# Performance work log

Measured on AMD Instinct MI355X. Metric: run time of the kernel, lower is better.

Reference implementation:

```python
import jax, jax.numpy as jnp
import numpy as np

W_EDGE, W_LAP, W_NORMAL, W_VEL = 0.5, 0.05, 0.01, 10.0


def _grid_mesh(g):
    ids = np.arange(g * g).reshape(g, g)
    tl, tr = ids[:-1, :-1].ravel(), ids[:-1, 1:].ravel()
    bl, br = ids[1:, :-1].ravel(), ids[1:, 1:].ravel()
    f1 = np.stack([tl, bl, br], 1)
    f2 = np.stack([tl, br, tr], 1)
    return np.concatenate([f1, f2], 0).astype(np.int64)  # [F,3]


def _topology(faces):
    # all directed edges with the opposite vertex of their face
    e = np.concatenate([faces[:, [0, 1]], faces[:, [1, 2]], faces[:, [2, 0]]], 0)
    opp = np.concatenate([faces[:, 2], faces[:, 0], faces[:, 1]], 0)
    key = np.sort(e, axis=1)
    uniq, inv = np.unique(key, axis=0, return_inverse=True)  # unique undirected edges
    counts = np.bincount(inv)
    order = np.argsort(inv, kind='stable')
    sel = counts[inv[order]] == 2
    idx2 = order[sel].reshape(-1, 2)  # the two face-slots of each interior edge
    ekey = key[idx2[:, 0]]
    pairs = np.stack([ekey[:, 0], ekey[:, 1], opp[idx2[:, 0]], opp[idx2[:, 1]]], 1)
    return uniq.astype(np.int64), pairs.astype(np.int64)


def setup_inputs() -> dict:
    key = jax.random.key(0)
    k1, k2 = jax.random.split(key)
    B, g = 2, 91
    N = g * g  # 8281
    faces = _grid_mesh(g)                 # [16200,3]
    edges, nc_pairs = _topology(faces)    # [24480,2], [24120,4]
    predictions = jax.random.normal(k1, (B, N, 3), dtype=jnp.float32)
    targets = jax.random.normal(k2, (B, N, 3), dtype=jnp.float32)
    return {
        'predictions': predictions,
        'targets': targets,
        'pred_faces': jnp.asarray(faces),
        'edges': jnp.asarray(edges),
        'nc_pairs': jnp.asarray(nc_pairs),
    }


def _chamfer(x, y):
    # pytorch3d chamfer_distance: squared dists, point mean both ways, batch mean
    xx = jnp.sum(x * x, -1)
    yy = jnp.sum(y * y, -1)
    d = xx[:, :, None] + yy[:, None, :] - 2.0 * jnp.einsum('bnd,bmd->bnm', x, y)
    d = jnp.maximum(d, 0.0)
    return jnp.mean(jnp.min(d, axis=2).mean(axis=1) + jnp.min(d, axis=1).mean(axis=1))


def _edge_loss(verts, edges):
    # mean over meshes of mean over edges of squared edge length (target len 0)
    ve = verts[:, edges]  # [B,E,2,3]
    l2 = jnp.sum((ve[:, :, 0] - ve[:, :, 1]) ** 2, -1)
    return l2.mean()


def _cot_laplacian_loss_one(verts, faces):
    # verts [N,3]; pytorch3d cot_laplacian + method='cot' smoothing
    fv = verts[faces]  # [F,3,3]
    v0, v1, v2 = fv[:, 0], fv[:, 1], fv[:, 2]
    A = jnp.linalg.norm(v1 - v2, axis=1)
    Bl = jnp.linalg.norm(v0 - v2, axis=1)
    C = jnp.linalg.norm(v0 - v1, axis=1)
    s = 0.5 * (A + Bl + C)
    area = jnp.sqrt(jnp.maximum(s * (s - A) * (s - Bl) * (s - C), 1e-12))
    A2, B2, C2 = A * A, Bl * Bl, C * C
    cota = (B2 + C2 - A2) / area
    cotb = (A2 + C2 - B2) / area
    cotc = (A2 + B2 - C2) / area
    cot = jnp.stack([cota, cotb, cotc], 1) / 4.0  # [F,3]
    ii = faces[:, jnp.array([1, 2, 0])]
    jj = faces[:, jnp.array([2, 0, 1])]
    i = jnp.concatenate([ii, jj], 0).ravel()
    j = jnp.concatenate([jj, ii], 0).ravel()
    w = jnp.concatenate([cot, cot], 0).ravel()
    N = verts.shape[0]
    Lx = jnp.zeros_like(verts).at[i].add(w[:, None] * verts[j])
    rowsum = jnp.zeros((N,), dtype=verts.dtype).at[i].add(w)
    norm_w = jnp.where(rowsum > 0, 1.0 / rowsum, 0.0)
    res = Lx * norm_w[:, None] - verts
    return jnp.linalg.norm(res, axis=1).mean()


def _normal_consistency_one(verts, pairs):
    # pairs [P,4] = (v0, v1, opp_a, opp_b) per interior edge
    p = verts[pairs]  # [P,4,3]
    e = p[:, 1] - p[:, 0]
    n0 = jnp.cross(e, p[:, 2] - p[:, 0])
    n1 = -jnp.cross(e, p[:, 3] - p[:, 0])
    eps = 1e-8
    cos = jnp.sum(n0 * n1, -1) / (
        jnp.maximum(jnp.linalg.norm(n0, axis=1), eps)
        * jnp.maximum(jnp.linalg.norm(n1, axis=1), eps)
    )
    return (1.0 - cos).mean()


def _forward(predictions, targets, pred_faces, edges, nc_pairs):
    loss_cham = _chamfer(predictions, targets)
    edge_l = _edge_loss(predictions, edges)
    lap_l = jax.vmap(lambda v: _cot_laplacian_loss_one(v, pred_faces))(predictions).mean()
    nc_l = jax.vmap(lambda v: _normal_consistency_one(v, nc_pairs))(predictions).mean()
    pred_shift = predictions[:, 1:, :] - predictions[:, :-1, :]
    tgt_shift = targets[:, 1:, :] - targets[:, :-1, :]
    vel_l = _chamfer(pred_shift, tgt_shift)
    return loss_cham + W_LAP * lap_l + W_NORMAL * nc_l + W_EDGE * edge_l + W_VEL * vel_l


def reference(predictions, targets, pred_faces, edges, nc_pairs):
    return _forward(predictions, targets, pred_faces, edges, nc_pairs)
```

## Files before the change

### kernel.cpp

```cpp
#include <hip/hip_runtime.h>


typedef unsigned int uint32;
typedef __attribute__((ext_vector_type(8)))  short bf16x8;
typedef __attribute__((ext_vector_type(16))) float f32x16;

#define W_EDGE   0.5f
#define W_LAP    0.05f
#define W_NORMAL 0.01f
#define W_VEL    10.0f
#define BIGF     3.0e38f
#define RSTRIDE  8320

__device__ __forceinline__ unsigned short f2bf(float f){
    uint32 b = __float_as_uint(f);
    b += 0x7FFFu + ((b >> 16) & 1u);
    return (unsigned short)(b >> 16);
}
__device__ __forceinline__ float bf2f(unsigned short h){
    return __uint_as_float(((uint32)h) << 16);
}

__device__ __forceinline__ float wave_sum(float v) {
#pragma unroll
    for (int o = 32; o > 0; o >>= 1) v += __shfl_down(v, o, 64);
    return v;
}

__global__ void bprep_k(const float* __restrict__ pred, const float* __restrict__ tgt,
                        int N, uint4* __restrict__ bfrag,
                        float* __restrict__ ws, int nzero)
{
    {
        uint32* w = (uint32*)ws;
        for (int i = blockIdx.x * blockDim.x + threadIdx.x; i < nzero;
             i += gridDim.x * blockDim.x)
            w[i] = 0u;
    }

    const int NT = (N + 31) >> 5;
    const int gt = blockIdx.x * 4 + (threadIdx.x >> 6);
    if (gt >= 8 * NT) return;
    const int c = gt / NT, t = gt - c * NT;
    const int dir = c >> 2, ds = (c >> 1) & 1, b = c & 1;
    const int Np = N - ds;
    const int l = threadIdx.x & 63;
    const int col = t * 32 + (l & 31);
    const float* __restrict__ yb = (dir ? pred : tgt) + (size_t)b * N * 3;
    float y0 = 0.f, y1 = 0.f, y2 = 0.f;
    const bool valid = col < Np;
    if (valid){
        if (ds){
            y0 = yb[(col+1)*3+0] - yb[col*3+0];
            y1 = yb[(col+1)*3+1] - yb[col*3+1];
            y2 = yb[(col+1)*3+2] - yb[col*3+2];
        } else {
            y0 = yb[col*3+0]; y1 = yb[col*3+1]; y2 = yb[col*3+2];
        }
    }
    const float yy = fmaf(y0,y0, fmaf(y1,y1, y2*y2));
    unsigned short yh0=f2bf(y0), yh1=f2bf(y1), yh2=f2bf(y2);
    unsigned short yl0=f2bf(y0-bf2f(yh0)), yl1=f2bf(y1-bf2f(yh1)), yl2=f2bf(y2-bf2f(yh2));
    unsigned short yyh, yyl;
    if (valid){ yyh = f2bf(yy); yyl = f2bf(yy - bf2f(yyh)); }
    else      { yyh = f2bf(BIGF); yyl = 0; }
    const short ONE = (short)0x3F80;
    bf16x8 Bu;
    if (l < 32){
        Bu[0]=(short)yh0; Bu[1]=(short)yh1; Bu[2]=(short)yh2;
        Bu[3]=(short)yh0; Bu[4]=(short)yh1; Bu[5]=(short)yh2;
        Bu[6]=(short)yl0; Bu[7]=(short)yl1;
    } else {
        Bu[0]=(short)yl2; Bu[1]=ONE; Bu[2]=ONE; Bu[3]=(short)yyh; Bu[4]=(short)yyl;
        Bu[5]=0; Bu[6]=0; Bu[7]=0;
    }
    bfrag[(size_t)(c * NT + t) * 64 + l] = __builtin_bit_cast(uint4, Bu);
}

__global__ __launch_bounds__(256)
void mega_k(const float* __restrict__ pred, const float* __restrict__ tgt,
            int N, const uint4* __restrict__ bfrag, float* __restrict__ rowpart,
            const int* __restrict__ edges, int E,
            const int* __restrict__ pairs, int P,
            const int* __restrict__ faces, int F,
            int B, float scaleE, float scaleP,
            float* __restrict__ Lx, float* __restrict__ rowsum,
            float* __restrict__ accum)
{
    if (blockIdx.z == 8){
        const int tE = B * E, tP = B * P, tF = B * F;
        const int total = tE + tP + tF;
        const int bid = blockIdx.x * 4 + blockIdx.y;
        const int nthr = 260 * 256;
        float se = 0.f, sp = 0.f;
        for (int idx = bid * 256 + threadIdx.x; idx < total; idx += nthr) {
            if (idx < tE) {
                const int b = idx / E;
                const int e = idx - b * E;
                const float* __restrict__ vb = pred + (size_t)b * N * 3;
                const int i0 = edges[e * 2 + 0], i1 = edges[e * 2 + 1];
                float dx = vb[i0 * 3 + 0] - vb[i1 * 3 + 0];
                float dy = vb[i0 * 3 + 1] - vb[i1 * 3 + 1];
                float dz = vb[i0 * 3 + 2] - vb[i1 * 3 + 2];
                se += fmaf(dx, dx, fmaf(dy, dy, dz * dz));
            } else if (idx < tE + tP) {
                const int q = idx - tE;
                const int b = q / P;
                const int p = q - b * P;
                const float* __restrict__ vb = pred + (size_t)b * N * 3;
                const int a0 = pairs[p * 4 + 0], a1 = pairs[p * 4 + 1];
                const int a2 = pairs[p * 4 + 2], a3 = pairs[p * 4 + 3];
                float p0x = vb[a0 * 3], p0y = vb[a0 * 3 + 1], p0z = vb[a0 * 3 + 2];
                float ex = vb[a1 * 3] - p0x, ey = vb[a1 * 3 + 1] - p0y, ez = vb[a1 * 3 + 2] - p0z;
                float ux = vb[a2 * 3] - p0x, uy = vb[a2 * 3 + 1] - p0y, uz = vb[a2 * 3 + 2] - p0z;
                float wx = vb[a3 * 3] - p0x, wy = vb[a3 * 3 + 1] - p0y, wz = vb[a3 * 3 + 2] - p0z;
                float n0x = ey * uz - ez * uy;
                float n0y = ez * ux - ex * uz;
                float n0z = ex * uy - ey * ux;
                float n1x = -(ey * wz - ez * wy);
                float n1y = -(ez * wx - ex * wz);
                float n1z = -(ex * wy - ey * wx);
                float dt = n0x * n1x + n0y * n1y + n0z * n1z;
                float l0 = sqrtf(n0x * n0x + n0y * n0y + n0z * n0z);
                float l1 = sqrtf(n1x * n1x + n1y * n1y + n1z * n1z);
                sp += 1.0f - dt / (fmaxf(l0, 1e-8f) * fmaxf(l1, 1e-8f));
            } else {
                const int q = idx - tE - tP;
                const int b = q / F;
                const int f = q - b * F;
                const float* __restrict__ vb = pred + (size_t)b * N * 3;
                const int i0 = faces[f * 3 + 0], i1 = faces[f * 3 + 1], i2 = faces[f * 3 + 2];
                float v0x = vb[i0 * 3], v0y = vb[i0 * 3 + 1], v0z = vb[i0 * 3 + 2];
                float v1x = vb[i1 * 3], v1y = vb[i1 * 3 + 1], v1z = vb[i1 * 3 + 2];
                float v2x = vb[i2 * 3], v2y = vb[i2 * 3 + 1], v2z = vb[i2 * 3 + 2];
                float ax = v1x - v2x, ay = v1y - v2y, az = v1z - v2z;
                float bx = v0x - v2x, by = v0y - v2y, bz = v0z - v2z;
                float cx = v0x - v1x, cy = v0y - v1y, cz = v0z - v1z;
                float A  = sqrtf(ax * ax + ay * ay + az * az);
                float Bl = sqrtf(bx * bx + by * by + bz * bz);
                float C  = sqrtf(cx * cx + cy * cy + cz * cz);
                float s2 = 0.5f * (A + Bl + C);
                float area = sqrtf(fmaxf(s2 * (s2 - A) * (s2 - Bl) * (s2 - C), 1e-12f));
                float A2 = A * A, B2 = Bl * Bl, C2 = C * C;
                float inv4a = 1.0f / (4.0f * area);
                float cota = (B2 + C2 - A2) * inv4a;
                float cotb = (A2 + C2 - B2) * inv4a;
                float cotc = (A2 + B2 - C2) * inv4a;

                float* __restrict__ Lb = Lx + (size_t)b * N * 3;
                float* __restrict__ rb = rowsum + (size_t)b * N;
                #define SCAT(i, j, wv)                                            \
                    atomicAdd(&Lb[(i) * 3 + 0], (wv) * vb[(j) * 3 + 0]);          \
                    atomicAdd(&Lb[(i) * 3 + 1], (wv) * vb[(j) * 3 + 1]);          \
                    atomicAdd(&Lb[(i) * 3 + 2], (wv) * vb[(j) * 3 + 2]);          \
                    atomicAdd(&rb[(i)], (wv));
                SCAT(i1, i2, cota) SCAT(i2, i1, cota)
                SCAT(i2, i0, cotb) SCAT(i0, i2, cotb)
                SCAT(i0, i1, cotc) SCAT(i1, i0, cotc)
                #undef SCAT
            }
        }
        se = wave_sum(se);
        sp = wave_sum(sp);
        if ((threadIdx.x & 63) == 0) atomicAdd(accum, fmaf(se, scaleE, sp * scaleP));
        return;
    }

    const int c = blockIdx.z;
    const int dir = c >> 2, ds = (c >> 1) & 1, b = c & 1;
    const int Np = N - ds;
    const int NT = (N + 31) >> 5;
    const int TC = (NT + 3) >> 2;
    const int t0 = blockIdx.y * TC;
    const int t1 = min(NT, t0 + TC);
    const int w = threadIdx.x >> 6, l = threadIdx.x & 63;
    const int h = l >> 5;
    const int grow = blockIdx.x * 128 + w * 32 + (l & 31);

    const float* __restrict__ xb = (dir ? tgt : pred) + (size_t)b * N * 3;
    float a0 = 0.f, a1 = 0.f, a2 = 0.f;
    const bool xvalid = grow < Np;
    if (xvalid){
        if (ds){
            a0 = xb[(grow+1)*3+0] - xb[grow*3+0];
            a1 = xb[(grow+1)*3+1] - xb[grow*3+1];
            a2 = xb[(grow+1)*3+2] - xb[grow*3+2];
        } else {
            a0 = xb[grow*3+0]; a1 = xb[grow*3+1]; a2 = xb[grow*3+2];
        }
    }
    const float xx = fmaf(a0,a0, fmaf(a1,a1, a2*a2));
    unsigned short xh0=f2bf(a0), xh1=f2bf(a1), xh2=f2bf(a2);
    unsigned short nxh0=f2bf(-2.f*bf2f(xh0)), nxh1=f2bf(-2.f*bf2f(xh1)), nxh2=f2bf(-2.f*bf2f(xh2));
    unsigned short nxl0=f2bf(-2.f*(a0-bf2f(xh0))), nxl1=f2bf(-2.f*(a1-bf2f(xh1))),
                   nxl2=f2bf(-2.f*(a2-bf2f(xh2)));
    unsigned short xxh=f2bf(xx), xxl=f2bf(xx-bf2f(xxh));
    const short ONE = (short)0x3F80;
    bf16x8 A;
    if (h == 0){
        A[0]=(short)nxh0; A[1]=(short)nxh1; A[2]=(short)nxh2;
        A[3]=(short)nxl0; A[4]=(short)nxl1; A[5]=(short)nxl2;
        A[6]=(short)nxh0; A[7]=(short)nxh1;
    } else {
        A[0]=(short)nxh2; A[1]=(short)xxh; A[2]=(short)xxl;
        A[3]=ONE; A[4]=ONE; A[5]=0; A[6]=0; A[7]=0;
    }

    f32x16 zacc;
#pragma unroll
    for (int r = 0; r < 16; ++r) zacc[r] = 0.f;
    float rm[16];
#pragma unroll
    for (int r = 0; r < 16; ++r) rm[r] = BIGF;

    const uint4* __restrict__ bfp = bfrag + (size_t)c * NT * 64 + l;

    const int ntile = t1 - t0;
    const int nb = ntile >> 3;

    int t = t0;
    for (int bt = 0; bt < nb; ++bt, t += 8){
        const uint4 T0 = bfp[(size_t)(t+0)*64];
        const uint4 T1 = bfp[(size_t)(t+1)*64];
        const uint4 T2 = bfp[(size_t)(t+2)*64];
        const uint4 T3 = bfp[(size_t)(t+3)*64];
        const uint4 T4 = bfp[(size_t)(t+4)*64];
        const uint4 T5 = bfp[(size_t)(t+5)*64];
        const uint4 T6 = bfp[(size_t)(t+6)*64];
        const uint4 T7 = bfp[(size_t)(t+7)*64];

        {
            const f32x16 u0 = __builtin_amdgcn_mfma_f32_32x32x16_bf16(
                A, __builtin_bit_cast(bf16x8, T0), zacc, 0, 0, 0);
            const f32x16 u1 = __builtin_amdgcn_mfma_f32_32x32x16_bf16(
                A, __builtin_bit_cast(bf16x8, T1), zacc, 0, 0, 0);
#pragma unroll
            for (int r = 0; r < 16; ++r) rm[r] = fminf(fminf(rm[r], u0[r]), u1[r]);
        }
        __builtin_amdgcn_sched_barrier(0);
        {
            const f32x16 u2 = __builtin_amdgcn_mfma_f32_32x32x16_bf16(
                A, __builtin_bit_cast(bf16x8, T2), zacc, 0, 0, 0);
            const f32x16 u3 = __builtin_amdgcn_mfma_f32_32x32x16_bf16(
                A, __builtin_bit_cast(bf16x8, T3), zacc, 0, 0, 0);
#pragma unroll
            for (int r = 0; r < 16; ++r) rm[r] = fminf(fminf(rm[r], u2[r]), u3[r]);
        }
        __builtin_amdgcn_sched_barrier(0);
        {
            const f32x16 u4 = __builtin_amdgcn_mfma_f32_32x32x16_bf16(
                A, __builtin_bit_cast(bf16x8, T4), zacc, 0, 0, 0);
            const f32x16 u5 = __builtin_amdgcn_mfma_f32_32x32x16_bf16(
                A, __builtin_bit_cast(bf16x8, T5), zacc, 0, 0, 0);
#pragma unroll
            for (int r = 0; r < 16; ++r) rm[r] = fminf(fminf(rm[r], u4[r]), u5[r]);
        }
        __builtin_amdgcn_sched_barrier(0);
        {
            const f32x16 u6 = __builtin_amdgcn_mfma_f32_32x32x16_bf16(
                A, __builtin_bit_cast(bf16x8, T6), zacc, 0, 0, 0);
            const f32x16 u7 = __builtin_amdgcn_mfma_f32_32x32x16_bf16(
                A, __builtin_bit_cast(bf16x8, T7), zacc, 0, 0, 0);
#pragma unroll
            for (int r = 0; r < 16; ++r) rm[r] = fminf(fminf(rm[r], u6[r]), u7[r]);
        }
        __builtin_amdgcn_sched_barrier(0);
    }
    for (; t < t1; ++t){
        const bf16x8 T0 = __builtin_bit_cast(bf16x8, bfp[(size_t)t * 64]);
        const f32x16 u0 = __builtin_amdgcn_mfma_f32_32x32x16_bf16(A, T0, zacc, 0, 0, 0);
#pragma unroll
        for (int r = 0; r < 16; ++r) rm[r] = fminf(rm[r], u0[r]);
    }

#pragma unroll
    for (int r = 0; r < 16; ++r){
        float v = rm[r];
        v = fminf(v, __shfl_xor(v, 1, 64));
        v = fminf(v, __shfl_xor(v, 2, 64));
        v = fminf(v, __shfl_xor(v, 4, 64));
        v = fminf(v, __shfl_xor(v, 8, 64));
        v = fminf(v, __shfl_xor(v, 16, 64));
        rm[r] = v;
    }
    float* __restrict__ rp = rowpart + (size_t)(c * 4 + blockIdx.y) * RSTRIDE;
#pragma unroll
    for (int r = 0; r < 16; ++r){
        if ((l & 31) == r){
            const int rowl = (r & 3) + 8 * (r >> 2) + 4 * h;
            const int gr = blockIdx.x * 128 + w * 32 + rowl;
            if (gr < Np) rp[gr] = rm[r];
        }
    }
}

__global__ void finalize_k(const float* __restrict__ rowpart,
                           const float* __restrict__ pred, const float* __restrict__ Lx,
                           const float* __restrict__ rowsum,
                           int N, float sMain, float sVel, float scaleL,
                           float* __restrict__ accum, float* __restrict__ out)
{
    const int total = 8 * N + 2 * N;
    float sm = 0.f, sv = 0.f, sl = 0.f;
    for (int idx = blockIdx.x * blockDim.x + threadIdx.x; idx < total;
         idx += gridDim.x * blockDim.x) {
        if (idx < 8 * N) {
            const int c = idx / N, i = idx - c * N;
            const int ds = (c >> 1) & 1;
            if (i < N - ds) {
                const float* rp = rowpart + (size_t)c * 4 * RSTRIDE;
                float v = fminf(fminf(rp[i], rp[RSTRIDE + i]),
                                fminf(rp[2*RSTRIDE + i], rp[3*RSTRIDE + i]));
                float d = fmaxf(v, 0.f);
                if (ds) sv += d; else sm += d;
            }
        } else {
            const int q = idx - 8 * N;
            float rs = rowsum[q];
            float nw = rs > 0.f ? 1.0f / rs : 0.f;
            float rx = Lx[q*3+0]*nw - pred[q*3+0];
            float ry = Lx[q*3+1]*nw - pred[q*3+1];
            float rz = Lx[q*3+2]*nw - pred[q*3+2];
            sl += sqrtf(rx*rx + ry*ry + rz*rz);
        }
    }
    sm = wave_sum(sm); sv = wave_sum(sv); sl = wave_sum(sl);
    if ((threadIdx.x & 63) == 0)
        atomicAdd(accum, fmaf(sm, sMain, fmaf(sv, sVel, sl * scaleL)));

    __syncthreads();
    if (threadIdx.x == 0){
        __threadfence();
        const uint32 prev = atomicAdd((uint32*)(accum + 4), 1u);
        if (prev == gridDim.x - 1)
            out[0] = atomicAdd(accum, 0.0f);
    }
}

extern "C" void kernel_launch(void* const* d_in, const int* in_sizes, int n_in,
                              void* d_out, int out_size, void* d_ws, size_t ws_size,
                              hipStream_t stream)
{
    const float* pred = (const float*)d_in[0];
    const float* tgt  = (const float*)d_in[1];
    const int* faces  = (const int*)d_in[2];
    const int* edges  = (const int*)d_in[3];
    const int* pairs  = (const int*)d_in[4];

    const int B = 2;
    const int N = in_sizes[0] / (3 * B);
    const int F = in_sizes[2] / 3;
    const int E = in_sizes[3] / 2;
    const int P = in_sizes[4] / 4;
    const int NT = (N + 31) >> 5;

    float* ws      = (float*)d_ws;
    float* accum   = ws;
    float* Lx      = ws + 8;
    float* rowsum  = Lx + (size_t)B * N * 3;
    float* rowpart = rowsum + (size_t)B * N;
    size_t off     = 8 + (size_t)B*N*3 + (size_t)B*N + (size_t)32*RSTRIDE;
    uint4* bfrag   = (uint4*)(ws + off);

    const int nzero = 8 + B * N * 3 + B * N;

    bprep_k<<<dim3((8 * NT + 3) / 4), dim3(256), 0, stream>>>(pred, tgt, N, bfrag,
                                                              ws, nzero);

    mega_k<<<dim3((N + 127) / 128, 4, 9), dim3(256), 0, stream>>>(
        pred, tgt, N, bfrag, rowpart,
        edges, E, pairs, P, faces, F, B,
        W_EDGE / ((float)B * (float)E),
        W_NORMAL / ((float)B * (float)P),
        Lx, rowsum, accum);

    finalize_k<<<96, dim3(256), 0, stream>>>(rowpart, pred, Lx, rowsum, N,
                                             1.0f / ((float)B * (float)N),
                                             W_VEL / ((float)B * (float)(N - 1)),
                                             W_LAP / ((float)B * (float)N),
                                             accum, (float*)d_out);
}
```

Measured before the change: 74.53 us.

## Split mesh losses into separate kernel and widen chamfer column chunks

Mesh-loss work (edge, normal consistency, cotangent scatter) moves out of the fused mega kernel's extra z-slice into its own 128-block kernel, launched after the chamfer kernel on the same stream. The chamfer MFMA kernel now splits the column tiles into 8 chunks instead of 4, doubling its grid so more CUs are busy. Finalize reduces over 8 partial row-min buffers instead of 4. The trade-offs are an extra launch, mesh work that no longer overlaps the chamfer work, and more partial-minimum traffic.

```diff
diff --git a/kernel.cpp b/kernel.cpp
--- a/kernel.cpp
+++ b/kernel.cpp
@@ -11,6 +11,7 @@
 #define W_VEL    10.0f
 #define BIGF     3.0e38f
 #define RSTRIDE  8320
+#define NCH      8
 
 __device__ __forceinline__ unsigned short f2bf(float f){
     uint32 b = __float_as_uint(f);
@@ -78,99 +79,15 @@
 }
 
 __global__ __launch_bounds__(256)
-void mega_k(const float* __restrict__ pred, const float* __restrict__ tgt,
-            int N, const uint4* __restrict__ bfrag, float* __restrict__ rowpart,
-            const int* __restrict__ edges, int E,
-            const int* __restrict__ pairs, int P,
-            const int* __restrict__ faces, int F,
-            int B, float scaleE, float scaleP,
-            float* __restrict__ Lx, float* __restrict__ rowsum,
-            float* __restrict__ accum)
-{
-    if (blockIdx.z == 8){
-        const int tE = B * E, tP = B * P, tF = B * F;
-        const int total = tE + tP + tF;
-        const int bid = blockIdx.x * 4 + blockIdx.y;
-        const int nthr = 260 * 256;
-        float se = 0.f, sp = 0.f;
-        for (int idx = bid * 256 + threadIdx.x; idx < total; idx += nthr) {
-            if (idx < tE) {
-                const int b = idx / E;
-                const int e = idx - b * E;
-                const float* __restrict__ vb = pred + (size_t)b * N * 3;
-                const int i0 = edges[e * 2 + 0], i1 = edges[e * 2 + 1];
-                float dx = vb[i0 * 3 + 0] - vb[i1 * 3 + 0];
-                float dy = vb[i0 * 3 + 1] - vb[i1 * 3 + 1];
-                float dz = vb[i0 * 3 + 2] - vb[i1 * 3 + 2];
-                se += fmaf(dx, dx, fmaf(dy, dy, dz * dz));
-            } else if (idx < tE + tP) {
-                const int q = idx - tE;
-                const int b = q / P;
-                const int p = q - b * P;
-                const float* __restrict__ vb = pred + (size_t)b * N * 3;
-                const int a0 = pairs[p * 4 + 0], a1 = pairs[p * 4 + 1];
-                const int a2 = pairs[p * 4 + 2], a3 = pairs[p * 4 + 3];
-                float p0x = vb[a0 * 3], p0y = vb[a0 * 3 + 1], p0z = vb[a0 * 3 + 2];
-                float ex = vb[a1 * 3] - p0x, ey = vb[a1 * 3 + 1] - p0y, ez = vb[a1 * 3 + 2] - p0z;
-                float ux = vb[a2 * 3] - p0x, uy = vb[a2 * 3 + 1] - p0y, uz = vb[a2 * 3 + 2] - p0z;
-                float wx = vb[a3 * 3] - p0x, wy = vb[a3 * 3 + 1] - p0y, wz = vb[a3 * 3 + 2] - p0z;
-                float n0x = ey * uz - ez * uy;
-                float n0y = ez * ux - ex * uz;
-                float n0z = ex * uy - ey * ux;
-                float n1x = -(ey * wz - ez * wy);
-                float n1y = -(ez * wx - ex * wz);
-                float n1z = -(ex * wy - ey * wx);
-                float dt = n0x * n1x + n0y * n1y + n0z * n1z;
-                float l0 = sqrtf(n0x * n0x + n0y * n0y + n0z * n0z);
-                float l1 = sqrtf(n1x * n1x + n1y * n1y + n1z * n1z);
-                sp += 1.0f - dt / (fmaxf(l0, 1e-8f) * fmaxf(l1, 1e-8f));
-            } else {
-                const int q = idx - tE - tP;
-                const int b = q / F;
-                const int f = q - b * F;
-                const float* __restrict__ vb = pred + (size_t)b * N * 3;
-                const int i0 = faces[f * 3 + 0], i1 = faces[f * 3 + 1], i2 = faces[f * 3 + 2];
-                float v0x = vb[i0 * 3], v0y = vb[i0 * 3 + 1], v0z = vb[i0 * 3 + 2];
-                float v1x = vb[i1 * 3], v1y = vb[i1 * 3 + 1], v1z = vb[i1 * 3 + 2];
-                float v2x = vb[i2 * 3], v2y = vb[i2 * 3 + 1], v2z = vb[i2 * 3 + 2];
-                float ax = v1x - v2x, ay = v1y - v2y, az = v1z - v2z;
-                float bx = v0x - v2x, by = v0y - v2y, bz = v0z - v2z;
-                float cx = v0x - v1x, cy = v0y - v1y, cz = v0z - v1z;
-                float A  = sqrtf(ax * ax + ay * ay + az * az);
-                float Bl = sqrtf(bx * bx + by * by + bz * bz);
-                float C  = sqrtf(cx * cx + cy * cy + cz * cz);
-                float s2 = 0.5f * (A + Bl + C);
-                float area = sqrtf(fmaxf(s2 * (s2 - A) * (s2 - Bl) * (s2 - C), 1e-12f));
-                float A2 = A * A, B2 = Bl * Bl, C2 = C * C;
-                float inv4a = 1.0f / (4.0f * area);
-                float cota = (B2 + C2 - A2) * inv4a;
-                float cotb = (A2 + C2 - B2) * inv4a;
-                float cotc = (A2 + B2 - C2) * inv4a;
-
-                float* __restrict__ Lb = Lx + (size_t)b * N * 3;
-                float* __restrict__ rb = rowsum + (size_t)b * N;
-                #define SCAT(i, j, wv)                                            \
-                    atomicAdd(&Lb[(i) * 3 + 0], (wv) * vb[(j) * 3 + 0]);          \
-                    atomicAdd(&Lb[(i) * 3 + 1], (wv) * vb[(j) * 3 + 1]);          \
-                    atomicAdd(&Lb[(i) * 3 + 2], (wv) * vb[(j) * 3 + 2]);          \
-                    atomicAdd(&rb[(i)], (wv));
-                SCAT(i1, i2, cota) SCAT(i2, i1, cota)
-                SCAT(i2, i0, cotb) SCAT(i0, i2, cotb)
-                SCAT(i0, i1, cotc) SCAT(i1, i0, cotc)
-                #undef SCAT
-            }
-        }
-        se = wave_sum(se);
-        sp = wave_sum(sp);
-        if ((threadIdx.x & 63) == 0) atomicAdd(accum, fmaf(se, scaleE, sp * scaleP));
-        return;
-    }
-
+void chamfer_mfma_k(const float* __restrict__ pred, const float* __restrict__ tgt,
+                    int N, const uint4* __restrict__ bfrag,
+                    float* __restrict__ rowpart)
+{
     const int c = blockIdx.z;
     const int dir = c >> 2, ds = (c >> 1) & 1, b = c & 1;
     const int Np = N - ds;
     const int NT = (N + 31) >> 5;
-    const int TC = (NT + 3) >> 2;
+    const int TC = (NT + NCH - 1) / NCH;
     const int t0 = blockIdx.y * TC;
     const int t1 = min(NT, t0 + TC);
     const int w = threadIdx.x >> 6, l = threadIdx.x & 63;
@@ -283,7 +200,7 @@
         v = fminf(v, __shfl_xor(v, 16, 64));
         rm[r] = v;
     }
-    float* __restrict__ rp = rowpart + (size_t)(c * 4 + blockIdx.y) * RSTRIDE;
+    float* __restrict__ rp = rowpart + (size_t)(c * NCH + blockIdx.y) * RSTRIDE;
 #pragma unroll
     for (int r = 0; r < 16; ++r){
         if ((l & 31) == r){
@@ -292,6 +209,90 @@
             if (gr < Np) rp[gr] = rm[r];
         }
     }
+}
+
+__global__ void mesh_k(const float* __restrict__ pred,
+                       const int* __restrict__ edges, int E,
+                       const int* __restrict__ pairs, int P,
+                       const int* __restrict__ faces, int F,
+                       int N, int B, float scaleE, float scaleP,
+                       float* __restrict__ Lx, float* __restrict__ rowsum,
+                       float* __restrict__ accum)
+{
+    const int tE = B * E, tP = B * P, tF = B * F;
+    const int total = tE + tP + tF;
+    float se = 0.f, sp = 0.f;
+    for (int idx = blockIdx.x * blockDim.x + threadIdx.x; idx < total;
+         idx += gridDim.x * blockDim.x) {
+        if (idx < tE) {
+            const int b = idx / E;
+            const int e = idx - b * E;
+            const float* __restrict__ vb = pred + (size_t)b * N * 3;
+            const int i0 = edges[e * 2 + 0], i1 = edges[e * 2 + 1];
+            float dx = vb[i0 * 3 + 0] - vb[i1 * 3 + 0];
+            float dy = vb[i0 * 3 + 1] - vb[i1 * 3 + 1];
+            float dz = vb[i0 * 3 + 2] - vb[i1 * 3 + 2];
+            se += fmaf(dx, dx, fmaf(dy, dy, dz * dz));
+        } else if (idx < tE + tP) {
+            const int q = idx - tE;
+            const int b = q / P;
+            const int p = q - b * P;
+            const float* __restrict__ vb = pred + (size_t)b * N * 3;
+            const int a0 = pairs[p * 4 + 0], a1 = pairs[p * 4 + 1];
+            const int a2 = pairs[p * 4 + 2], a3 = pairs[p * 4 + 3];
+            float p0x = vb[a0 * 3], p0y = vb[a0 * 3 + 1], p0z = vb[a0 * 3 + 2];
+            float ex = vb[a1 * 3] - p0x, ey = vb[a1 * 3 + 1] - p0y, ez = vb[a1 * 3 + 2] - p0z;
+            float ux = vb[a2 * 3] - p0x, uy = vb[a2 * 3 + 1] - p0y, uz = vb[a2 * 3 + 2] - p0z;
+            float wx = vb[a3 * 3] - p0x, wy = vb[a3 * 3 + 1] - p0y, wz = vb[a3 * 3 + 2] - p0z;
+            float n0x = ey * uz - ez * uy;
+            float n0y = ez * ux - ex * uz;
+            float n0z = ex * uy - ey * ux;
+            float n1x = -(ey * wz - ez * wy);
+            float n1y = -(ez * wx - ex * wz);
+            float n1z = -(ex * wy - ey * wx);
+            float dt = n0x * n1x + n0y * n1y + n0z * n1z;
+            float l0 = sqrtf(n0x * n0x + n0y * n0y + n0z * n0z);
+            float l1 = sqrtf(n1x * n1x + n1y * n1y + n1z * n1z);
+            sp += 1.0f - dt / (fmaxf(l0, 1e-8f) * fmaxf(l1, 1e-8f));
+        } else {
+            const int q = idx - tE - tP;
+            const int b = q / F;
+            const int f = q - b * F;
+            const float* __restrict__ vb = pred + (size_t)b * N * 3;
+            const int i0 = faces[f * 3 + 0], i1 = faces[f * 3 + 1], i2 = faces[f * 3 + 2];
+            float v0x = vb[i0 * 3], v0y = vb[i0 * 3 + 1], v0z = vb[i0 * 3 + 2];
+            float v1x = vb[i1 * 3], v1y = vb[i1 * 3 + 1], v1z = vb[i1 * 3 + 2];
+            float v2x = vb[i2 * 3], v2y = vb[i2 * 3 + 1], v2z = vb[i2 * 3 + 2];
+            float ax = v1x - v2x, ay = v1y - v2y, az = v1z - v2z;
+            float bx = v0x - v2x, by = v0y - v2y, bz = v0z - v2z;
+            float cx = v0x - v1x, cy = v0y - v1y, cz = v0z - v1z;
+            float A  = sqrtf(ax * ax + ay * ay + az * az);
+            float Bl = sqrtf(bx * bx + by * by + bz * bz);
+            float C  = sqrtf(cx * cx + cy * cy + cz * cz);
+            float s2 = 0.5f * (A + Bl + C);
+            float area = sqrtf(fmaxf(s2 * (s2 - A) * (s2 - Bl) * (s2 - C), 1e-12f));
+            float A2 = A * A, B2 = Bl * Bl, C2 = C * C;
+            float inv4a = 1.0f / (4.0f * area);
+            float cota = (B2 + C2 - A2) * inv4a;
+            float cotb = (A2 + C2 - B2) * inv4a;
+            float cotc = (A2 + B2 - C2) * inv4a;
+
+            float* __restrict__ Lb = Lx + (size_t)b * N * 3;
+            float* __restrict__ rb = rowsum + (size_t)b * N;
+            #define SCAT(i, j, wv)                                            \
+                atomicAdd(&Lb[(i) * 3 + 0], (wv) * vb[(j) * 3 + 0]);          \
+                atomicAdd(&Lb[(i) * 3 + 1], (wv) * vb[(j) * 3 + 1]);          \
+                atomicAdd(&Lb[(i) * 3 + 2], (wv) * vb[(j) * 3 + 2]);          \
+                atomicAdd(&rb[(i)], (wv));
+            SCAT(i1, i2, cota) SCAT(i2, i1, cota)
+            SCAT(i2, i0, cotb) SCAT(i0, i2, cotb)
+            SCAT(i0, i1, cotc) SCAT(i1, i0, cotc)
+            #undef SCAT
+        }
+    }
+    se = wave_sum(se);
+    sp = wave_sum(sp);
+    if ((threadIdx.x & 63) == 0) atomicAdd(accum, fmaf(se, scaleE, sp * scaleP));
 }
 
 __global__ void finalize_k(const float* __restrict__ rowpart,
@@ -308,9 +309,11 @@
             const int c = idx / N, i = idx - c * N;
             const int ds = (c >> 1) & 1;
             if (i < N - ds) {
-                const float* rp = rowpart + (size_t)c * 4 * RSTRIDE;
-                float v = fminf(fminf(rp[i], rp[RSTRIDE + i]),
-                                fminf(rp[2*RSTRIDE + i], rp[3*RSTRIDE + i]));
+                const float* rp = rowpart + (size_t)c * NCH * RSTRIDE;
+                float v = BIGF;
+#pragma unroll
+                for (int k = 0; k < NCH; ++k)
+                    v = fminf(v, rp[(size_t)k * RSTRIDE + i]);
                 float d = fmaxf(v, 0.f);
                 if (ds) sv += d; else sm += d;
             }
@@ -359,7 +362,7 @@
     float* Lx      = ws + 8;
     float* rowsum  = Lx + (size_t)B * N * 3;
     float* rowpart = rowsum + (size_t)B * N;
-    size_t off     = 8 + (size_t)B*N*3 + (size_t)B*N + (size_t)32*RSTRIDE;
+    size_t off     = 8 + (size_t)B*N*3 + (size_t)B*N + (size_t)8*NCH*RSTRIDE;
     uint4* bfrag   = (uint4*)(ws + off);
 
     const int nzero = 8 + B * N * 3 + B * N;
@@ -367,12 +370,13 @@
     bprep_k<<<dim3((8 * NT + 3) / 4), dim3(256), 0, stream>>>(pred, tgt, N, bfrag,
                                                               ws, nzero);
 
-    mega_k<<<dim3((N + 127) / 128, 4, 9), dim3(256), 0, stream>>>(
-        pred, tgt, N, bfrag, rowpart,
-        edges, E, pairs, P, faces, F, B,
-        W_EDGE / ((float)B * (float)E),
-        W_NORMAL / ((float)B * (float)P),
-        Lx, rowsum, accum);
+    chamfer_mfma_k<<<dim3((N + 127) / 128, NCH, 8), dim3(256), 0, stream>>>(
+        pred, tgt, N, bfrag, rowpart);
+
+    mesh_k<<<128, dim3(256), 0, stream>>>(pred, edges, E, pairs, P, faces, F, N, B,
+                                          W_EDGE / ((float)B * (float)E),
+                                          W_NORMAL / ((float)B * (float)P),
+                                          Lx, rowsum, accum);
 
     finalize_k<<<96, dim3(256), 0, stream>>>(rowpart, pred, Lx, rowsum, N,
                                              1.0f / ((float)B * (float)N),
```

Result: slower. 89.28 us (+19.8%).
